# Kernel optimization log

Hardware: AMD Instinct MI355X
Metric: run time of the kernel (lower is better)

Reference implementation:

```python
import jax, jax.numpy as jnp
import numpy as np

IN_DIM = 128
MEM_DIM = 256
NUM_CLASSES = 12
NUM_LEVELS = 17  # complete binary tree, N = 2**17 - 1 = 131071 nodes


def setup_inputs() -> dict:
    key = jax.random.key(0)
    ks = jax.random.split(key, 7)
    N = 2 ** NUM_LEVELS - 1
    s = 1.0 / np.sqrt(MEM_DIM)  # PyTorch LSTMCell/Linear init scale
    return {
        "x": jax.random.normal(ks[0], (N, IN_DIM), dtype=jnp.float32),
        "W_ih": jax.random.uniform(ks[1], (4 * MEM_DIM, IN_DIM), jnp.float32, -s, s),
        "b_ih": jax.random.uniform(ks[2], (4 * MEM_DIM,), jnp.float32, -s, s),
        "W_hh": jax.random.uniform(ks[3], (4 * MEM_DIM, MEM_DIM), jnp.float32, -s, s),
        "b_hh": jax.random.uniform(ks[4], (4 * MEM_DIM,), jnp.float32, -s, s),
        "W_fc": jax.random.uniform(ks[5], (NUM_CLASSES, MEM_DIM), jnp.float32, -s, s),
        "b_fc": jax.random.uniform(ks[6], (NUM_CLASSES,), jnp.float32, -s, s),
        "num_levels": NUM_LEVELS,
    }


def reference(x, W_ih, b_ih, W_hh, b_hh, W_fc, b_fc, num_levels):
    # Complete binary tree in BFS order: level l occupies nodes [2^l-1, 2^(l+1)-2];
    # children of level-l nodes are exactly the (contiguous) level-(l+1) nodes.
    mem = W_hh.shape[1]
    h_below = None
    c_below = None
    for l in reversed(range(num_levels)):
        n = 2 ** l
        x_l = x[n - 1:2 * n - 1]  # [n, in_dim] nodes at this level
        if h_below is None:  # leaves: zero child state
            ch_h = jnp.zeros((n, mem), dtype=x.dtype)
            ch_c = ch_h
        else:  # sum the two children's (h, c), as the recursion accumulates
            ch_h = h_below.reshape(n, 2, mem).sum(axis=1)
            ch_c = c_below.reshape(n, 2, mem).sum(axis=1)
        # PyTorch LSTMCell: gates = x W_ih^T + b_ih + h W_hh^T + b_hh, chunks i,f,g,o
        gates = x_l @ W_ih.T + b_ih + ch_h @ W_hh.T + b_hh  # [n, 4*mem]
        i, f, g, o = jnp.split(gates, 4, axis=-1)
        c_new = jax.nn.sigmoid(f) * ch_c + jax.nn.sigmoid(i) * jnp.tanh(g)
        h_new = jax.nn.sigmoid(o) * jnp.tanh(c_new)
        h_below, c_below = h_new, c_new
    # Original applies FC to state[1] == cell state c of the root (kept faithfully).
    return c_below[:1] @ W_fc.T + b_fc  # [1, num_classes]
```

## Files before the change

kernel.cpp:

```cpp
#include <hip/hip_runtime.h>
#include <hip/hip_bf16.h>
#include <cstddef>

#define IN_DIM 128
#define MEM 256
#define KTOT 384
#define NLEAF 65536
#define TAIL_TOP 6
#define NBLK_TAIL 8

typedef float f32x4 __attribute__((ext_vector_type(4)));
typedef short s16x8 __attribute__((ext_vector_type(8)));
typedef unsigned int u32;

__device__ inline unsigned short f2bf(float f){
    unsigned int u = __builtin_bit_cast(unsigned int, f);
    u += 0x7fff + ((u >> 16) & 1);
    return (unsigned short)(u >> 16);
}

__device__ inline void gld_lds16(const void* g, void* l){
    __builtin_amdgcn_global_load_lds((const __attribute__((address_space(1))) u32*)g,
                                     (__attribute__((address_space(3))) u32*)l, 16, 0, 0);
}

__device__ inline float fsigm(float x){
    return __builtin_amdgcn_rcpf(1.f + __expf(-x));
}
__device__ inline float ftanh(float x){
    return 2.f * __builtin_amdgcn_rcpf(1.f + __expf(-2.f * x)) - 1.f;
}

__host__ __device__ inline size_t offA(int l){
    if (l == 16) return 0;
    return 8388608u + 384u * (65536u - (1u << (l + 1)));
}
#define ARENA_ELEMS 33554048u
#define ARENA_PAD   65536u

__device__ inline void grid_barrier(unsigned* ctr, unsigned target){
    __syncthreads();
    if (threadIdx.x == 0){
        __threadfence();
        __hip_atomic_fetch_add(ctr, 1u, __ATOMIC_RELEASE, __HIP_MEMORY_SCOPE_AGENT);
        while (__hip_atomic_load(ctr, __ATOMIC_ACQUIRE, __HIP_MEMORY_SCOPE_AGENT) < target)
            __builtin_amdgcn_s_sleep(1);
    }
    __syncthreads();
    __threadfence();
}

__global__ void pack_w_kernel(const float* __restrict__ W_ih, const float* __restrict__ b_ih,
                              const float* __restrict__ W_hh, const float* __restrict__ b_hh,
                              unsigned short* __restrict__ Wp, float* __restrict__ bp,
                              unsigned* __restrict__ ctr){
    int row = blockIdx.x;
    for (int k = threadIdx.x; k < KTOT; k += blockDim.x){
        float v = (k < IN_DIM) ? W_ih[row * IN_DIM + k] : W_hh[row * MEM + (k - IN_DIM)];
        Wp[row * KTOT + k] = f2bf(v);
    }
    if (threadIdx.x == 0){
        bp[row] = b_ih[row] + b_hh[row];
        if (row == 0) *ctr = 0;
    }
}

__global__ void pack_x_kernel(const float* __restrict__ x, unsigned short* __restrict__ Aarena){
    const int TOTAL_G = 131071 * 16;
    for (int g = blockIdx.x * blockDim.x + threadIdx.x; g < TOTAL_G; g += gridDim.x * blockDim.x){
        int i  = g >> 4;
        int ko = (g & 15) * 8;
        int l  = 31 - __clz(i + 1);
        int j  = i + 1 - (1 << l);
        size_t dst = offA(l) + (size_t)j * ((l == 16) ? 128 : 384) + ko;
        const f32x4* s = (const f32x4*)(x + (size_t)i * IN_DIM + ko);
        f32x4 v0 = s[0], v1 = s[1];
        s16x8 o;
        #pragma unroll
        for (int e = 0; e < 4; ++e){ o[e] = (short)f2bf(v0[e]); o[4+e] = (short)f2bf(v1[e]); }
        *(s16x8*)(Aarena + dst) = o;
    }
}

#define BM 128
#define KC 64

template<int NK>
__global__ __launch_bounds__(256) void gemm_lstm_kernel(
    const unsigned short* __restrict__ A, int n,
    const unsigned short* __restrict__ Wp, const float* __restrict__ bp,
    const float* __restrict__ csum_in, int leaf,
    unsigned short* __restrict__ A_next, float* __restrict__ csum_out)
{
    __shared__ __align__(16) unsigned short As[2][BM * KC];
    __shared__ __align__(16) unsigned short Bs[2][BM * KC];

    const int tid  = threadIdx.x;
    const int lane = tid & 63;
    const int wid  = tid >> 6;
    const int wm   = wid >> 1;
    const int wc   = wid & 1;
    const int row0 = blockIdx.x * BM;
    const int m0   = blockIdx.y * 32;

    const int srow = lane >> 3;
    const int scol = ((lane & 7) ^ srow) * 8;

    const int mg = m0 + wc * 16 + (lane & 15);

    const float b0 = bp[0 * 256 + mg];
    const float b1 = bp[1 * 256 + mg];
    const float b2 = bp[2 * 256 + mg];
    const float b3 = bp[3 * 256 + mg];
    float cpre[4][4];
    if (!leaf){
        #pragma unroll
        for (int r = 0; r < 4; ++r){
            const int base = row0 + wm * 64 + r * 16 + (lane >> 4) * 4;
            #pragma unroll
            for (int e = 0; e < 4; ++e)
                cpre[r][e] = csum_in[(size_t)(base + e) * MEM + mg];
        }
    } else {
        #pragma unroll
        for (int r = 0; r < 4; ++r)
            #pragma unroll
            for (int e = 0; e < 4; ++e) cpre[r][e] = 0.f;
    }

    f32x4 acc[4][4];
    #pragma unroll
    for (int r = 0; r < 4; ++r)
        #pragma unroll
        for (int q = 0; q < 4; ++q)
            acc[r][q] = (f32x4){0.f, 0.f, 0.f, 0.f};

    auto stage = [&](int d, int kk){
        char* asb = (char*)As[d];
        char* bsb = (char*)Bs[d];
        #pragma unroll
        for (int q = 0; q < 4; ++q){
            int t = wid * 4 + q;
            int r = t * 8 + srow;
            gld_lds16(A + (size_t)(row0 + r) * NK + kk + scol, asb + t * 1024);
        }
        #pragma unroll
        for (int q = 0; q < 4; ++q){
            int t = wid * 4 + q;
            int b = t * 8 + srow;
            int grow = (b >> 5) * 256 + m0 + (b & 31);
            gld_lds16(Wp + (size_t)grow * KTOT + kk + scol, bsb + t * 1024);
        }
    };

    constexpr int nIter = NK / KC;
    stage(0, 0);
    int buf = 0;
    #pragma unroll
    for (int it = 0; it < nIter; ++it){
        if (it + 1 < nIter){
            stage(buf ^ 1, (it + 1) * KC);
            asm volatile("s_waitcnt vmcnt(8)" ::: "memory");
        } else {
            asm volatile("s_waitcnt vmcnt(0)" ::: "memory");
        }
        __builtin_amdgcn_s_barrier();
        const unsigned short* Ab = As[buf];
        const unsigned short* Bb = Bs[buf];
        #pragma unroll
        for (int ks = 0; ks < 2; ++ks){
            const int slot = ks * 4 + (lane >> 4);
            const int kb = (slot ^ (lane & 7)) * 8;
            s16x8 a[4], b[4];
            #pragma unroll
            for (int r = 0; r < 4; ++r)
                a[r] = *(const s16x8*)(Ab + (wm * 64 + r * 16 + (lane & 15)) * KC + kb);
            #pragma unroll
            for (int q = 0; q < 4; ++q)
                b[q] = *(const s16x8*)(Bb + (q * 32 + wc * 16 + (lane & 15)) * KC + kb);
            #pragma unroll
            for (int r = 0; r < 4; ++r)
                #pragma unroll
                for (int q = 0; q < 4; ++q)
                    acc[r][q] = __builtin_amdgcn_mfma_f32_16x16x32_bf16(a[r], b[q], acc[r][q], 0, 0, 0);
        }
        __builtin_amdgcn_s_barrier();
        buf ^= 1;
    }

    #pragma unroll
    for (int r = 0; r < 4; ++r){
        const int base = row0 + wm * 64 + r * 16 + (lane >> 4) * 4;
        float cn[4], hn[4];
        #pragma unroll
        for (int e = 0; e < 4; ++e){
            float iv = acc[r][0][e] + b0;
            float fv = acc[r][1][e] + b1;
            float gv = acc[r][2][e] + b2;
            float ov = acc[r][3][e] + b3;
            float c  = fsigm(fv) * cpre[r][e] + fsigm(iv) * ftanh(gv);
            cn[e] = c;
            hn[e] = fsigm(ov) * ftanh(c);
        }
        if (base < n){
            int p0 = base >> 1;
            A_next[(size_t)p0 * KTOT + IN_DIM + mg] = f2bf(hn[0] + hn[1]);
            csum_out[(size_t)p0 * MEM + mg] = cn[0] + cn[1];
        }
        if (base + 2 < n){
            int p1 = (base >> 1) + 1;
            A_next[(size_t)p1 * KTOT + IN_DIM + mg] = f2bf(hn[2] + hn[3]);
            csum_out[(size_t)p1 * MEM + mg] = cn[2] + cn[3];
        }
    }
}

__global__ __launch_bounds__(256) void tail_kernel(
    const unsigned short* __restrict__ arena,
    const unsigned short* __restrict__ Wp, const float* __restrict__ bp,
    float* cs_in, float* cs_out,
    float* __restrict__ c_root,
    const float* __restrict__ W_fc, const float* __restrict__ b_fc,
    float* __restrict__ out, unsigned* __restrict__ ctr)
{
    __shared__ __align__(16) unsigned short WpL[128 * KTOT];
    __shared__ __align__(16) unsigned short AL[64 * KTOT];

    const int tid  = threadIdx.x;
    const int lane = tid & 63;
    const int wid  = tid >> 6;
    const int wm   = wid >> 1;
    const int wc   = wid & 1;
    const int m0   = blockIdx.x * 32;
    const int mg   = m0 + wc * 16 + (lane & 15);

    #pragma unroll
    for (int i = 0; i < 24; ++i){
        int p0 = wid * 1536 + i * 64;
        int p  = p0 + lane;
        int lrow  = p / 48;
        int pslot = p % 48;
        int lslot = pslot ^ (lrow & 7);
        int grow  = (lrow >> 5) * 256 + m0 + (lrow & 31);
        gld_lds16(Wp + (size_t)grow * KTOT + lslot * 8, (char*)WpL + (size_t)p0 * 16);
    }

    const float b0 = bp[0 * 256 + mg];
    const float b1 = bp[1 * 256 + mg];
    const float b2 = bp[2 * 256 + mg];
    const float b3 = bp[3 * 256 + mg];

    asm volatile("s_waitcnt vmcnt(0)" ::: "memory");
    __builtin_amdgcn_s_barrier();

    unsigned gen = 0;
    for (int l = TAIL_TOP; l >= 0; --l){
        const int n = 1 << l;
        const unsigned short* Al = arena + offA(l);

        const int nslots = n * 48;
        for (int t = 0; t * 256 < nslots; ++t){
            int pbase = t * 256 + wid * 64;
            int p = pbase + lane;
            if (p < nslots){
                int row   = p / 48;
                int pslot = p - row * 48;
                int lslot = pslot ^ (row & 7);
                gld_lds16(Al + (size_t)row * KTOT + lslot * 8, (char*)AL + (size_t)pbase * 16);
            }
        }

        float cpre[2][4];
        #pragma unroll
        for (int r = 0; r < 2; ++r){
            const int base = wm * 32 + r * 16 + (lane >> 4) * 4;
            #pragma unroll
            for (int e = 0; e < 4; ++e)
                cpre[r][e] = cs_in[(size_t)(base + e) * MEM + mg];
        }

        asm volatile("s_waitcnt vmcnt(0)" ::: "memory");
        __builtin_amdgcn_s_barrier();

        f32x4 acc[2][4];
        #pragma unroll
        for (int r = 0; r < 2; ++r)
            #pragma unroll
            for (int q = 0; q < 4; ++q)
                acc[r][q] = (f32x4){0.f, 0.f, 0.f, 0.f};

        #pragma unroll
        for (int kc = 0; kc < 12; ++kc){
            const int ls = kc * 4 + (lane >> 4);
            const int kb = (ls ^ (lane & 7)) * 8;
            s16x8 a[2], b[4];
            #pragma unroll
            for (int r = 0; r < 2; ++r)
                a[r] = *(const s16x8*)(AL + (size_t)(wm * 32 + r * 16 + (lane & 15)) * KTOT + kb);
            #pragma unroll
            for (int q = 0; q < 4; ++q)
                b[q] = *(const s16x8*)(WpL + (q * 32 + wc * 16 + (lane & 15)) * KTOT + kb);
            #pragma unroll
            for (int r = 0; r < 2; ++r)
                #pragma unroll
                for (int q = 0; q < 4; ++q)
                    acc[r][q] = __builtin_amdgcn_mfma_f32_16x16x32_bf16(a[r], b[q], acc[r][q], 0, 0, 0);
        }

        #pragma unroll
        for (int r = 0; r < 2; ++r){
            const int base = wm * 32 + r * 16 + (lane >> 4) * 4;
            float cn[4], hn[4];
            #pragma unroll
            for (int e = 0; e < 4; ++e){
                float iv = acc[r][0][e] + b0;
                float fv = acc[r][1][e] + b1;
                float gv = acc[r][2][e] + b2;
                float ov = acc[r][3][e] + b3;
                float c  = fsigm(fv) * cpre[r][e] + fsigm(iv) * ftanh(gv);
                cn[e] = c;
                hn[e] = fsigm(ov) * ftanh(c);
            }
            if (l == 0){
                if (base == 0) c_root[mg] = cn[0];
            } else {
                unsigned short* A_next = (unsigned short*)arena + offA(l - 1);
                if (base < n){
                    int p0 = base >> 1;
                    A_next[(size_t)p0 * KTOT + IN_DIM + mg] = f2bf(hn[0] + hn[1]);
                    cs_out[(size_t)p0 * MEM + mg] = cn[0] + cn[1];
                }
                if (base + 2 < n){
                    int p1 = (base >> 1) + 1;
                    A_next[(size_t)p1 * KTOT + IN_DIM + mg] = f2bf(hn[2] + hn[3]);
                    cs_out[(size_t)p1 * MEM + mg] = cn[2] + cn[3];
                }
            }
        }
        float* t = cs_in; cs_in = cs_out; cs_out = t;
        ++gen;
        grid_barrier(ctr, (unsigned)(NBLK_TAIL * gen));
    }

    if (blockIdx.x == 0){
        int w = wid;
        for (int cls = w * 3; cls < w * 3 + 3; ++cls){
            float s = 0.f;
            for (int m = lane; m < 256; m += 64)
                s += c_root[m] * W_fc[cls * 256 + m];
            #pragma unroll
            for (int off = 32; off; off >>= 1)
                s += __shfl_down(s, off, 64);
            if (lane == 0) out[cls] = s + b_fc[cls];
        }
    }
}

extern "C" void kernel_launch(void* const* d_in, const int* in_sizes, int n_in,
                              void* d_out, int out_size, void* d_ws, size_t ws_size,
                              hipStream_t stream)
{
    const float* x    = (const float*)d_in[0];
    const float* W_ih = (const float*)d_in[1];
    const float* b_ih = (const float*)d_in[2];
    const float* W_hh = (const float*)d_in[3];
    const float* b_hh = (const float*)d_in[4];
    const float* W_fc = (const float*)d_in[5];
    const float* b_fc = (const float*)d_in[6];
    float* out = (float*)d_out;

    const size_t OFF_WP = 0;
    const size_t OFF_BP = 786432;
    const size_t OFF_A  = 790528;
    const size_t OFF_CS0 = OFF_A + (size_t)(ARENA_ELEMS + ARENA_PAD) * 2;
    const size_t OFF_CS1 = OFF_CS0 + 33554432;
    const size_t OFF_CR  = OFF_CS1 + 33554432;
    const size_t OFF_CTR = OFF_CR + 1024;
    const size_t NEEDED  = OFF_CTR + 64;
    if (ws_size < NEEDED) return;

    char* ws = (char*)d_ws;
    unsigned short* Wp    = (unsigned short*)(ws + OFF_WP);
    float* bp             = (float*)(ws + OFF_BP);
    unsigned short* arena = (unsigned short*)(ws + OFF_A);
    float* cs0            = (float*)(ws + OFF_CS0);
    float* cs1            = (float*)(ws + OFF_CS1);
    float* c_root         = (float*)(ws + OFF_CR);
    unsigned* ctr         = (unsigned*)(ws + OFF_CTR);

    pack_w_kernel<<<dim3(1024), dim3(128), 0, stream>>>(W_ih, b_ih, W_hh, b_hh, Wp, bp, ctr);
    pack_x_kernel<<<dim3(2048), dim3(256), 0, stream>>>(x, arena);

    gemm_lstm_kernel<IN_DIM><<<dim3(NLEAF / BM, 8), dim3(256), 0, stream>>>(
        arena + offA(16), NLEAF, Wp, bp,
        nullptr, 1, arena + offA(15), cs0);

    float* cs_in = cs0; float* cs_out = cs1;
    for (int l = 15; l >= 7; --l){
        int n = 1 << l;
        gemm_lstm_kernel<KTOT><<<dim3(n / BM, 8), dim3(256), 0, stream>>>(
            arena + offA(l), n, Wp, bp,
            cs_in, 0, arena + offA(l - 1), cs_out);
        float* t = cs_in; cs_in = cs_out; cs_out = t;
    }

    tail_kernel<<<dim3(NBLK_TAIL), dim3(256), 0, stream>>>(
        arena, Wp, bp, cs_in, cs_out, c_root, W_fc, b_fc, out, ctr);
}
```

Before: 224.1 us.

## Use 256x256 tiles with 512-thread blocks for the large-level LSTM GEMMs

Adds a GEMM+LSTM kernel that uses a 256-row by 256-gate-column tile (64 per gate) per 512-thread block and double-buffered LDS, used for the leaf level and levels 15..8. Level 7 keeps the old 128-row kernel because it has only 128 rows. The larger tiles should raise MFMA work per loaded byte and halve the number of blocks. In exchange the kernel uses more LDS and registers per block, and the smaller levels get fewer blocks, which lowers occupancy there.

```diff
diff --git a/kernel.cpp b/kernel.cpp
--- a/kernel.cpp
+++ b/kernel.cpp
@@ -79,6 +79,124 @@
         #pragma unroll
         for (int e = 0; e < 4; ++e){ o[e] = (short)f2bf(v0[e]); o[4+e] = (short)f2bf(v1[e]); }
         *(s16x8*)(Aarena + dst) = o;
+    }
+}
+
+template<int NK>
+__global__ __launch_bounds__(512, 2) void gemm_lstm256_kernel(
+    const unsigned short* __restrict__ A, int n,
+    const unsigned short* __restrict__ Wp, const float* __restrict__ bp,
+    const float* __restrict__ csum_in, int leaf,
+    unsigned short* __restrict__ A_next, float* __restrict__ csum_out)
+{
+    __shared__ __align__(16) unsigned short As[2][256 * 64];
+    __shared__ __align__(16) unsigned short Bs[2][256 * 64];
+
+    const int tid  = threadIdx.x;
+    const int lane = tid & 63;
+    const int wid  = tid >> 6;
+    const int wm   = wid >> 2;
+    const int wn   = wid & 3;
+    const int row0 = blockIdx.x * 256;
+    const int m0   = blockIdx.y * 64;
+
+    f32x4 acc[8][4];
+    #pragma unroll
+    for (int r = 0; r < 8; ++r)
+        #pragma unroll
+        for (int q = 0; q < 4; ++q)
+            acc[r][q] = (f32x4){0.f, 0.f, 0.f, 0.f};
+
+    auto stage = [&](int d, int kk){
+        #pragma unroll
+        for (int i = 0; i < 4; ++i){
+            int p   = i * 512 + tid;
+            int row = p >> 3;
+            int ls  = (p & 7) ^ (row & 7);
+            gld_lds16(A + (size_t)(row0 + row) * NK + kk + ls * 8, (char*)As[d] + (size_t)p * 16);
+        }
+        #pragma unroll
+        for (int i = 0; i < 4; ++i){
+            int p   = i * 512 + tid;
+            int b   = p >> 3;
+            int ls  = (p & 7) ^ (b & 7);
+            int grow = (b >> 6) * 256 + m0 + (b & 63);
+            gld_lds16(Wp + (size_t)grow * KTOT + kk + ls * 8, (char*)Bs[d] + (size_t)p * 16);
+        }
+    };
+
+    constexpr int nkt = NK / 64;
+    stage(0, 0);
+    stage(1, 64);
+
+    #pragma unroll
+    for (int kt = 0; kt < nkt; ++kt){
+        const int buf = kt & 1;
+        if (kt < nkt - 1){
+            asm volatile("s_waitcnt vmcnt(8)" ::: "memory");
+        } else {
+            asm volatile("s_waitcnt vmcnt(0)" ::: "memory");
+        }
+        __builtin_amdgcn_s_barrier();
+
+        const unsigned short* Ab = As[buf];
+        const unsigned short* Bb = Bs[buf];
+        #pragma unroll
+        for (int ks = 0; ks < 2; ++ks){
+            const int ls = ks * 4 + (lane >> 4);
+            const int kb = (ls ^ (lane & 7)) * 8;
+            s16x8 bfr[4];
+            #pragma unroll
+            for (int q = 0; q < 4; ++q)
+                bfr[q] = *(const s16x8*)(Bb + (size_t)(q * 64 + wn * 16 + (lane & 15)) * 64 + kb);
+            #pragma unroll
+            for (int rh = 0; rh < 2; ++rh){
+                s16x8 a[4];
+                #pragma unroll
+                for (int j = 0; j < 4; ++j)
+                    a[j] = *(const s16x8*)(Ab + (size_t)(wm * 128 + (rh * 4 + j) * 16 + (lane & 15)) * 64 + kb);
+                #pragma unroll
+                for (int j = 0; j < 4; ++j)
+                    #pragma unroll
+                    for (int q = 0; q < 4; ++q)
+                        acc[rh * 4 + j][q] = __builtin_amdgcn_mfma_f32_16x16x32_bf16(a[j], bfr[q], acc[rh * 4 + j][q], 0, 0, 0);
+            }
+        }
+
+        if (kt + 2 < nkt){
+            __builtin_amdgcn_s_barrier();
+            stage(buf, (kt + 2) * 64);
+        }
+    }
+
+    const int mg = m0 + wn * 16 + (lane & 15);
+    const float b0 = bp[0 * 256 + mg];
+    const float b1 = bp[1 * 256 + mg];
+    const float b2 = bp[2 * 256 + mg];
+    const float b3 = bp[3 * 256 + mg];
+    #pragma unroll
+    for (int r = 0; r < 8; ++r){
+        const int base = row0 + wm * 128 + r * 16 + (lane >> 4) * 4;
+        float cpre[4];
+        #pragma unroll
+        for (int e = 0; e < 4; ++e)
+            cpre[e] = leaf ? 0.f : csum_in[(size_t)(base + e) * MEM + mg];
+        float cn[4], hn[4];
+        #pragma unroll
+        for (int e = 0; e < 4; ++e){
+            float iv = acc[r][0][e] + b0;
+            float fv = acc[r][1][e] + b1;
+            float gv = acc[r][2][e] + b2;
+            float ov = acc[r][3][e] + b3;
+            float c  = fsigm(fv) * cpre[e] + fsigm(iv) * ftanh(gv);
+            cn[e] = c;
+            hn[e] = fsigm(ov) * ftanh(c);
+        }
+        int p0 = base >> 1;
+        A_next[(size_t)p0 * KTOT + IN_DIM + mg] = f2bf(hn[0] + hn[1]);
+        csum_out[(size_t)p0 * MEM + mg] = cn[0] + cn[1];
+        A_next[(size_t)(p0 + 1) * KTOT + IN_DIM + mg] = f2bf(hn[2] + hn[3]);
+        csum_out[(size_t)(p0 + 1) * MEM + mg] = cn[2] + cn[3];
     }
 }
 
@@ -391,19 +509,24 @@
     pack_w_kernel<<<dim3(1024), dim3(128), 0, stream>>>(W_ih, b_ih, W_hh, b_hh, Wp, bp, ctr);
     pack_x_kernel<<<dim3(2048), dim3(256), 0, stream>>>(x, arena);
 
-    gemm_lstm_kernel<IN_DIM><<<dim3(NLEAF / BM, 8), dim3(256), 0, stream>>>(
+    gemm_lstm256_kernel<IN_DIM><<<dim3(NLEAF / 256, 4), dim3(512), 0, stream>>>(
         arena + offA(16), NLEAF, Wp, bp,
         nullptr, 1, arena + offA(15), cs0);
 
     float* cs_in = cs0; float* cs_out = cs1;
-    for (int l = 15; l >= 7; --l){
+    for (int l = 15; l >= 8; --l){
         int n = 1 << l;
-        gemm_lstm_kernel<KTOT><<<dim3(n / BM, 8), dim3(256), 0, stream>>>(
+        gemm_lstm256_kernel<KTOT><<<dim3(n >> 8, 4), dim3(512), 0, stream>>>(
             arena + offA(l), n, Wp, bp,
             cs_in, 0, arena + offA(l - 1), cs_out);
         float* t = cs_in; cs_in = cs_out; cs_out = t;
     }
 
+    gemm_lstm_kernel<KTOT><<<dim3(1, 8), dim3(256), 0, stream>>>(
+        arena + offA(7), 128, Wp, bp,
+        cs_in, 0, arena + offA(6), cs_out);
+    { float* t = cs_in; cs_in = cs_out; cs_out = t; }
+
     tail_kernel<<<dim3(NBLK_TAIL), dim3(256), 0, stream>>>(
         arena, Wp, bp, cs_in, cs_out, c_root, W_fc, b_fc, out, ctr);
 }
```

Result: slower. 280.7 us (+25.3%).

## Fuse mid tree levels into persistent kernel with grid barriers and merge pack kernels

Applied to the files above, without the earlier changes.

Levels 12 down to 7, which were separate small GEMM+LSTM launches, now run inside one persistent 256-block kernel that steps through them with a global atomic barrier between levels. This removes several kernel launch gaps and tail effects on levels that are too small to fill the GPU. The weight and x packing kernels are also merged into one launch, with a second counter slot set aside for the tail kernel. The persistent kernel relies on all 256 blocks being co-resident, and the spin barrier adds its own cost at each level.

```diff
diff --git a/kernel.cpp b/kernel.cpp
--- a/kernel.cpp
+++ b/kernel.cpp
@@ -8,6 +8,7 @@
 #define NLEAF 65536
 #define TAIL_TOP 6
 #define NBLK_TAIL 8
+#define NBLK_MID 256
 
 typedef float f32x4 __attribute__((ext_vector_type(4)));
 typedef short s16x8 __attribute__((ext_vector_type(8)));
@@ -50,24 +51,29 @@
     __threadfence();
 }
 
-__global__ void pack_w_kernel(const float* __restrict__ W_ih, const float* __restrict__ b_ih,
-                              const float* __restrict__ W_hh, const float* __restrict__ b_hh,
-                              unsigned short* __restrict__ Wp, float* __restrict__ bp,
-                              unsigned* __restrict__ ctr){
-    int row = blockIdx.x;
-    for (int k = threadIdx.x; k < KTOT; k += blockDim.x){
-        float v = (k < IN_DIM) ? W_ih[row * IN_DIM + k] : W_hh[row * MEM + (k - IN_DIM)];
-        Wp[row * KTOT + k] = f2bf(v);
-    }
-    if (threadIdx.x == 0){
-        bp[row] = b_ih[row] + b_hh[row];
-        if (row == 0) *ctr = 0;
-    }
-}
-
-__global__ void pack_x_kernel(const float* __restrict__ x, unsigned short* __restrict__ Aarena){
+__global__ void pack_kernel(const float* __restrict__ x,
+                            const float* __restrict__ W_ih, const float* __restrict__ b_ih,
+                            const float* __restrict__ W_hh, const float* __restrict__ b_hh,
+                            unsigned short* __restrict__ Wp, float* __restrict__ bp,
+                            unsigned short* __restrict__ Aarena, unsigned* __restrict__ ctr){
+    const int stride = gridDim.x * blockDim.x;
+    const int tid0 = blockIdx.x * blockDim.x + threadIdx.x;
+    if (tid0 == 0){ ctr[0] = 0; ctr[16] = 0; }
+
+    for (int g = tid0; g < 1024 * 48; g += stride){
+        int row = g / 48, ko = (g - row * 48) * 8;
+        const float* s = (ko < IN_DIM) ? (W_ih + (size_t)row * IN_DIM + ko)
+                                       : (W_hh + (size_t)row * MEM + (ko - IN_DIM));
+        f32x4 v0 = *(const f32x4*)s, v1 = *(const f32x4*)(s + 4);
+        s16x8 o;
+        #pragma unroll
+        for (int e = 0; e < 4; ++e){ o[e] = (short)f2bf(v0[e]); o[4+e] = (short)f2bf(v1[e]); }
+        *(s16x8*)(Wp + (size_t)row * KTOT + ko) = o;
+        if (ko == 0) bp[row] = b_ih[row] + b_hh[row];
+    }
+
     const int TOTAL_G = 131071 * 16;
-    for (int g = blockIdx.x * blockDim.x + threadIdx.x; g < TOTAL_G; g += gridDim.x * blockDim.x){
+    for (int g = tid0; g < TOTAL_G; g += stride){
         int i  = g >> 4;
         int ko = (g & 15) * 8;
         int l  = 31 - __clz(i + 1);
@@ -86,22 +92,19 @@
 #define KC 64
 
 template<int NK>
-__global__ __launch_bounds__(256) void gemm_lstm_kernel(
+__device__ __forceinline__ void gemm128_body(
     const unsigned short* __restrict__ A, int n,
     const unsigned short* __restrict__ Wp, const float* __restrict__ bp,
     const float* __restrict__ csum_in, int leaf,
-    unsigned short* __restrict__ A_next, float* __restrict__ csum_out)
+    unsigned short* __restrict__ A_next, float* __restrict__ csum_out,
+    int row0, int m0,
+    unsigned short (&As)[2][BM * KC], unsigned short (&Bs)[2][BM * KC])
 {
-    __shared__ __align__(16) unsigned short As[2][BM * KC];
-    __shared__ __align__(16) unsigned short Bs[2][BM * KC];
-
     const int tid  = threadIdx.x;
     const int lane = tid & 63;
     const int wid  = tid >> 6;
     const int wm   = wid >> 1;
     const int wc   = wid & 1;
-    const int row0 = blockIdx.x * BM;
-    const int m0   = blockIdx.y * 32;
 
     const int srow = lane >> 3;
     const int scol = ((lane & 7) ^ srow) * 8;
@@ -212,6 +215,43 @@
             A_next[(size_t)p1 * KTOT + IN_DIM + mg] = f2bf(hn[2] + hn[3]);
             csum_out[(size_t)p1 * MEM + mg] = cn[2] + cn[3];
         }
+    }
+}
+
+template<int NK>
+__global__ __launch_bounds__(256) void gemm_lstm_kernel(
+    const unsigned short* __restrict__ A, int n,
+    const unsigned short* __restrict__ Wp, const float* __restrict__ bp,
+    const float* __restrict__ csum_in, int leaf,
+    unsigned short* __restrict__ A_next, float* __restrict__ csum_out)
+{
+    __shared__ __align__(16) unsigned short As[2][BM * KC];
+    __shared__ __align__(16) unsigned short Bs[2][BM * KC];
+    gemm128_body<NK>(A, n, Wp, bp, csum_in, leaf, A_next, csum_out,
+                     blockIdx.x * BM, blockIdx.y * 32, As, Bs);
+}
+
+__global__ __launch_bounds__(256) void mid_kernel(
+    unsigned short* __restrict__ arena,
+    const unsigned short* __restrict__ Wp, const float* __restrict__ bp,
+    float* cs_a, float* cs_b, unsigned* __restrict__ ctr)
+{
+    __shared__ __align__(16) unsigned short As[2][BM * KC];
+    __shared__ __align__(16) unsigned short Bs[2][BM * KC];
+    const int rb = blockIdx.x >> 3;
+    const int m0 = (blockIdx.x & 7) * 32;
+
+    float* cs_in = cs_a; float* cs_out = cs_b;
+    unsigned gen = 0;
+    for (int l = 12; l >= 7; --l){
+        const int n = 1 << l;
+        if (rb < (n >> 7)){
+            gemm128_body<KTOT>(arena + offA(l), n, Wp, bp, cs_in, 0,
+                               arena + offA(l - 1), cs_out, rb * BM, m0, As, Bs);
+        }
+        float* t = cs_in; cs_in = cs_out; cs_out = t;
+        ++gen;
+        grid_barrier(ctr, (unsigned)(NBLK_MID * gen));
     }
 }
 
@@ -376,7 +416,7 @@
     const size_t OFF_CS1 = OFF_CS0 + 33554432;
     const size_t OFF_CR  = OFF_CS1 + 33554432;
     const size_t OFF_CTR = OFF_CR + 1024;
-    const size_t NEEDED  = OFF_CTR + 64;
+    const size_t NEEDED  = OFF_CTR + 128;
     if (ws_size < NEEDED) return;
 
     char* ws = (char*)d_ws;
@@ -388,22 +428,23 @@
     float* c_root         = (float*)(ws + OFF_CR);
     unsigned* ctr         = (unsigned*)(ws + OFF_CTR);
 
-    pack_w_kernel<<<dim3(1024), dim3(128), 0, stream>>>(W_ih, b_ih, W_hh, b_hh, Wp, bp, ctr);
-    pack_x_kernel<<<dim3(2048), dim3(256), 0, stream>>>(x, arena);
+    pack_kernel<<<dim3(2048), dim3(256), 0, stream>>>(
+        x, W_ih, b_ih, W_hh, b_hh, Wp, bp, arena, ctr);
 
     gemm_lstm_kernel<IN_DIM><<<dim3(NLEAF / BM, 8), dim3(256), 0, stream>>>(
         arena + offA(16), NLEAF, Wp, bp,
         nullptr, 1, arena + offA(15), cs0);
 
-    float* cs_in = cs0; float* cs_out = cs1;
-    for (int l = 15; l >= 7; --l){
-        int n = 1 << l;
-        gemm_lstm_kernel<KTOT><<<dim3(n / BM, 8), dim3(256), 0, stream>>>(
-            arena + offA(l), n, Wp, bp,
-            cs_in, 0, arena + offA(l - 1), cs_out);
-        float* t = cs_in; cs_in = cs_out; cs_out = t;
-    }
+    gemm_lstm_kernel<KTOT><<<dim3(256, 8), dim3(256), 0, stream>>>(
+        arena + offA(15), 32768, Wp, bp, cs0, 0, arena + offA(14), cs1);
+    gemm_lstm_kernel<KTOT><<<dim3(128, 8), dim3(256), 0, stream>>>(
+        arena + offA(14), 16384, Wp, bp, cs1, 0, arena + offA(13), cs0);
+    gemm_lstm_kernel<KTOT><<<dim3(64, 8), dim3(256), 0, stream>>>(
+        arena + offA(13), 8192, Wp, bp, cs0, 0, arena + offA(12), cs1);
+
+    mid_kernel<<<dim3(NBLK_MID), dim3(256), 0, stream>>>(
+        arena, Wp, bp, cs1, cs0, ctr);
 
     tail_kernel<<<dim3(NBLK_TAIL), dim3(256), 0, stream>>>(
-        arena, Wp, bp, cs_in, cs_out, c_root, W_fc, b_fc, out, ctr);
-}
+        arena, Wp, bp, cs1, cs0, c_root, W_fc, b_fc, out, ctr + 16);
+}
```

New measurement: 492.3 us. 120% more time.

## Merge pack kernels and fold level 7 into persistent tail kernel

Applied to the files above, without the earlier changes.

Combines the weight and input packing kernels into one launch with vectorized weight conversion. Moves tree level 7 from a separate GEMM launch into the persistent tail kernel, which now processes a level in 64-row chunks when n exceeds 64. The grid barrier spin uses a relaxed load and a longer sleep. The aim is fewer kernel launches and less launch overhead, at the cost of running level 7 on only 8 blocks instead of a full grid.

```diff
diff --git a/kernel.cpp b/kernel.cpp
--- a/kernel.cpp
+++ b/kernel.cpp
@@ -6,7 +6,6 @@
 #define MEM 256
 #define KTOT 384
 #define NLEAF 65536
-#define TAIL_TOP 6
 #define NBLK_TAIL 8
 
 typedef float f32x4 __attribute__((ext_vector_type(4)));
@@ -43,31 +42,36 @@
     if (threadIdx.x == 0){
         __threadfence();
         __hip_atomic_fetch_add(ctr, 1u, __ATOMIC_RELEASE, __HIP_MEMORY_SCOPE_AGENT);
-        while (__hip_atomic_load(ctr, __ATOMIC_ACQUIRE, __HIP_MEMORY_SCOPE_AGENT) < target)
-            __builtin_amdgcn_s_sleep(1);
+        while (__hip_atomic_load(ctr, __ATOMIC_RELAXED, __HIP_MEMORY_SCOPE_AGENT) < target)
+            __builtin_amdgcn_s_sleep(2);
     }
     __syncthreads();
     __threadfence();
 }
 
-__global__ void pack_w_kernel(const float* __restrict__ W_ih, const float* __restrict__ b_ih,
-                              const float* __restrict__ W_hh, const float* __restrict__ b_hh,
-                              unsigned short* __restrict__ Wp, float* __restrict__ bp,
-                              unsigned* __restrict__ ctr){
-    int row = blockIdx.x;
-    for (int k = threadIdx.x; k < KTOT; k += blockDim.x){
-        float v = (k < IN_DIM) ? W_ih[row * IN_DIM + k] : W_hh[row * MEM + (k - IN_DIM)];
-        Wp[row * KTOT + k] = f2bf(v);
-    }
-    if (threadIdx.x == 0){
-        bp[row] = b_ih[row] + b_hh[row];
-        if (row == 0) *ctr = 0;
-    }
-}
-
-__global__ void pack_x_kernel(const float* __restrict__ x, unsigned short* __restrict__ Aarena){
+__global__ void pack_kernel(const float* __restrict__ x,
+                            const float* __restrict__ W_ih, const float* __restrict__ b_ih,
+                            const float* __restrict__ W_hh, const float* __restrict__ b_hh,
+                            unsigned short* __restrict__ Wp, float* __restrict__ bp,
+                            unsigned short* __restrict__ Aarena, unsigned* __restrict__ ctr){
+    const int stride = gridDim.x * blockDim.x;
+    const int tid0 = blockIdx.x * blockDim.x + threadIdx.x;
+    if (tid0 == 0){ ctr[0] = 0; }
+
+    for (int g = tid0; g < 1024 * 48; g += stride){
+        int row = g / 48, ko = (g - row * 48) * 8;
+        const float* s = (ko < IN_DIM) ? (W_ih + (size_t)row * IN_DIM + ko)
+                                       : (W_hh + (size_t)row * MEM + (ko - IN_DIM));
+        f32x4 v0 = *(const f32x4*)s, v1 = *(const f32x4*)(s + 4);
+        s16x8 o;
+        #pragma unroll
+        for (int e = 0; e < 4; ++e){ o[e] = (short)f2bf(v0[e]); o[4+e] = (short)f2bf(v1[e]); }
+        *(s16x8*)(Wp + (size_t)row * KTOT + ko) = o;
+        if (ko == 0) bp[row] = b_ih[row] + b_hh[row];
+    }
+
     const int TOTAL_G = 131071 * 16;
-    for (int g = blockIdx.x * blockDim.x + threadIdx.x; g < TOTAL_G; g += gridDim.x * blockDim.x){
+    for (int g = tid0; g < TOTAL_G; g += stride){
         int i  = g >> 4;
         int ko = (g & 15) * 8;
         int l  = 31 - __clz(i + 1);
@@ -254,89 +258,98 @@
     __builtin_amdgcn_s_barrier();
 
     unsigned gen = 0;
-    for (int l = TAIL_TOP; l >= 0; --l){
+    for (int l = 7; l >= 0; --l){
         const int n = 1 << l;
         const unsigned short* Al = arena + offA(l);
-
-        const int nslots = n * 48;
-        for (int t = 0; t * 256 < nslots; ++t){
-            int pbase = t * 256 + wid * 64;
-            int p = pbase + lane;
-            if (p < nslots){
-                int row   = p / 48;
-                int pslot = p - row * 48;
-                int lslot = pslot ^ (row & 7);
-                gld_lds16(Al + (size_t)row * KTOT + lslot * 8, (char*)AL + (size_t)pbase * 16);
-            }
-        }
-
-        float cpre[2][4];
-        #pragma unroll
-        for (int r = 0; r < 2; ++r){
-            const int base = wm * 32 + r * 16 + (lane >> 4) * 4;
-            #pragma unroll
-            for (int e = 0; e < 4; ++e)
-                cpre[r][e] = cs_in[(size_t)(base + e) * MEM + mg];
-        }
-
-        asm volatile("s_waitcnt vmcnt(0)" ::: "memory");
-        __builtin_amdgcn_s_barrier();
-
-        f32x4 acc[2][4];
-        #pragma unroll
-        for (int r = 0; r < 2; ++r)
-            #pragma unroll
-            for (int q = 0; q < 4; ++q)
-                acc[r][q] = (f32x4){0.f, 0.f, 0.f, 0.f};
-
-        #pragma unroll
-        for (int kc = 0; kc < 12; ++kc){
-            const int ls = kc * 4 + (lane >> 4);
-            const int kb = (ls ^ (lane & 7)) * 8;
-            s16x8 a[2], b[4];
-            #pragma unroll
-            for (int r = 0; r < 2; ++r)
-                a[r] = *(const s16x8*)(AL + (size_t)(wm * 32 + r * 16 + (lane & 15)) * KTOT + kb);
-            #pragma unroll
-            for (int q = 0; q < 4; ++q)
-                b[q] = *(const s16x8*)(WpL + (q * 32 + wc * 16 + (lane & 15)) * KTOT + kb);
-            #pragma unroll
-            for (int r = 0; r < 2; ++r)
-                #pragma unroll
-                for (int q = 0; q < 4; ++q)
-                    acc[r][q] = __builtin_amdgcn_mfma_f32_16x16x32_bf16(a[r], b[q], acc[r][q], 0, 0, 0);
-        }
-
-        #pragma unroll
-        for (int r = 0; r < 2; ++r){
-            const int base = wm * 32 + r * 16 + (lane >> 4) * 4;
-            float cn[4], hn[4];
-            #pragma unroll
-            for (int e = 0; e < 4; ++e){
-                float iv = acc[r][0][e] + b0;
-                float fv = acc[r][1][e] + b1;
-                float gv = acc[r][2][e] + b2;
-                float ov = acc[r][3][e] + b3;
-                float c  = fsigm(fv) * cpre[r][e] + fsigm(iv) * ftanh(gv);
-                cn[e] = c;
-                hn[e] = fsigm(ov) * ftanh(c);
-            }
-            if (l == 0){
-                if (base == 0) c_root[mg] = cn[0];
-            } else {
-                unsigned short* A_next = (unsigned short*)arena + offA(l - 1);
-                if (base < n){
-                    int p0 = base >> 1;
-                    A_next[(size_t)p0 * KTOT + IN_DIM + mg] = f2bf(hn[0] + hn[1]);
-                    cs_out[(size_t)p0 * MEM + mg] = cn[0] + cn[1];
-                }
-                if (base + 2 < n){
-                    int p1 = (base >> 1) + 1;
-                    A_next[(size_t)p1 * KTOT + IN_DIM + mg] = f2bf(hn[2] + hn[3]);
-                    cs_out[(size_t)p1 * MEM + mg] = cn[2] + cn[3];
+        const int nhalf = (n > 64) ? (n >> 6) : 1;
+
+        for (int h = 0; h < nhalf; ++h){
+            const int r0 = h * 64;
+            const int rows = (n < 64) ? n : 64;
+
+            const int nslots = rows * 48;
+            for (int t = 0; t * 256 < nslots; ++t){
+                int pbase = t * 256 + wid * 64;
+                int p = pbase + lane;
+                if (p < nslots){
+                    int row   = p / 48;
+                    int pslot = p - row * 48;
+                    int lslot = pslot ^ (row & 7);
+                    gld_lds16(Al + (size_t)(r0 + row) * KTOT + lslot * 8,
+                              (char*)AL + (size_t)pbase * 16);
                 }
             }
-        }
+
+            float cpre[2][4];
+            #pragma unroll
+            for (int r = 0; r < 2; ++r){
+                const int base = r0 + wm * 32 + r * 16 + (lane >> 4) * 4;
+                #pragma unroll
+                for (int e = 0; e < 4; ++e)
+                    cpre[r][e] = cs_in[(size_t)(base + e) * MEM + mg];
+            }
+
+            asm volatile("s_waitcnt vmcnt(0)" ::: "memory");
+            __builtin_amdgcn_s_barrier();
+
+            f32x4 acc[2][4];
+            #pragma unroll
+            for (int r = 0; r < 2; ++r)
+                #pragma unroll
+                for (int q = 0; q < 4; ++q)
+                    acc[r][q] = (f32x4){0.f, 0.f, 0.f, 0.f};
+
+            #pragma unroll
+            for (int kc = 0; kc < 12; ++kc){
+                const int ls = kc * 4 + (lane >> 4);
+                const int kb = (ls ^ (lane & 7)) * 8;
+                s16x8 a[2], b[4];
+                #pragma unroll
+                for (int r = 0; r < 2; ++r)
+                    a[r] = *(const s16x8*)(AL + (size_t)(wm * 32 + r * 16 + (lane & 15)) * KTOT + kb);
+                #pragma unroll
+                for (int q = 0; q < 4; ++q)
+                    b[q] = *(const s16x8*)(WpL + (q * 32 + wc * 16 + (lane & 15)) * KTOT + kb);
+                #pragma unroll
+                for (int r = 0; r < 2; ++r)
+                    #pragma unroll
+                    for (int q = 0; q < 4; ++q)
+                        acc[r][q] = __builtin_amdgcn_mfma_f32_16x16x32_bf16(a[r], b[q], acc[r][q], 0, 0, 0);
+            }
+
+            #pragma unroll
+            for (int r = 0; r < 2; ++r){
+                const int base = r0 + wm * 32 + r * 16 + (lane >> 4) * 4;
+                float cn[4], hn[4];
+                #pragma unroll
+                for (int e = 0; e < 4; ++e){
+                    float iv = acc[r][0][e] + b0;
+                    float fv = acc[r][1][e] + b1;
+                    float gv = acc[r][2][e] + b2;
+                    float ov = acc[r][3][e] + b3;
+                    float c  = fsigm(fv) * cpre[r][e] + fsigm(iv) * ftanh(gv);
+                    cn[e] = c;
+                    hn[e] = fsigm(ov) * ftanh(c);
+                }
+                if (l == 0){
+                    if (base == 0) c_root[mg] = cn[0];
+                } else {
+                    unsigned short* A_next = (unsigned short*)arena + offA(l - 1);
+                    if (base < n){
+                        int p0 = base >> 1;
+                        A_next[(size_t)p0 * KTOT + IN_DIM + mg] = f2bf(hn[0] + hn[1]);
+                        cs_out[(size_t)p0 * MEM + mg] = cn[0] + cn[1];
+                    }
+                    if (base + 2 < n){
+                        int p1 = (base >> 1) + 1;
+                        A_next[(size_t)p1 * KTOT + IN_DIM + mg] = f2bf(hn[2] + hn[3]);
+                        cs_out[(size_t)p1 * MEM + mg] = cn[2] + cn[3];
+                    }
+                }
+            }
+            __builtin_amdgcn_s_barrier();
+        }
+
         float* t = cs_in; cs_in = cs_out; cs_out = t;
         ++gen;
         grid_barrier(ctr, (unsigned)(NBLK_TAIL * gen));
@@ -388,15 +401,15 @@
     float* c_root         = (float*)(ws + OFF_CR);
     unsigned* ctr         = (unsigned*)(ws + OFF_CTR);
 
-    pack_w_kernel<<<dim3(1024), dim3(128), 0, stream>>>(W_ih, b_ih, W_hh, b_hh, Wp, bp, ctr);
-    pack_x_kernel<<<dim3(2048), dim3(256), 0, stream>>>(x, arena);
+    pack_kernel<<<dim3(2048), dim3(256), 0, stream>>>(
+        x, W_ih, b_ih, W_hh, b_hh, Wp, bp, arena, ctr);
 
     gemm_lstm_kernel<IN_DIM><<<dim3(NLEAF / BM, 8), dim3(256), 0, stream>>>(
         arena + offA(16), NLEAF, Wp, bp,
         nullptr, 1, arena + offA(15), cs0);
 
     float* cs_in = cs0; float* cs_out = cs1;
-    for (int l = 15; l >= 7; --l){
+    for (int l = 15; l >= 8; --l){
         int n = 1 << l;
         gemm_lstm_kernel<KTOT><<<dim3(n / BM, 8), dim3(256), 0, stream>>>(
             arena + offA(l), n, Wp, bp,
```

After: 220.4 us. No clear change (-1.6%).
